# Performance work log

Hardware: AMD Instinct MI355X
Metric: run time of the kernel (lower is better)

## Reference

```python
import jax, jax.numpy as jnp
import numpy as np

N, T, F, H, DEG = 1024, 32, 128, 4, 32
HID, OUT = 512, 64
NNZ = N * DEG
D = F // H


def setup_inputs() -> dict:
    key = jax.random.key(0)
    ks = jax.random.split(key, 40)
    p = lambda i, shape, s=0.05: (jax.random.normal(ks[i], shape, dtype=jnp.float32) * s)
    inp = {
        'A_rows': jnp.repeat(jnp.arange(N, dtype=jnp.int32), DEG),
        'A_cols': jax.random.randint(ks[0], (NNZ,), 0, N, dtype=jnp.int32),
        'A_vals': jax.random.uniform(ks[1], (NNZ,), dtype=jnp.float32) / DEG,
        'X': jax.random.normal(ks[2], (N, T, F), dtype=jnp.float32),
        'W_gcn': p(3, (F, F)),
        'W_ih': p(4, (3 * F, F)), 'W_hh': p(5, (3 * F, F)),
        'b_ih': p(6, (3 * F,)), 'b_hh': p(7, (3 * F,)),
        'in_proj_w': p(8, (3 * F, F)), 'in_proj_b': p(9, (3 * F,)),
        'out_proj_w': p(10, (F, F)), 'out_proj_b': p(11, (F,)),
        'ln1_g': jnp.ones((F,), jnp.float32), 'ln1_b': jnp.zeros((F,), jnp.float32),
        'ln2_g': jnp.ones((F,), jnp.float32), 'ln2_b': jnp.zeros((F,), jnp.float32),
        'lnf_g': jnp.ones((F,), jnp.float32), 'lnf_b': jnp.zeros((F,), jnp.float32),
        'ff1_w': p(12, (HID, F)), 'ff1_b': p(13, (HID,)),
        'ff2_w': p(14, (F, HID)), 'ff2_b': p(15, (F,)),
        'fc1_w': p(16, (HID, T * F)), 'fc1_b': p(17, (HID,)),
        'fc2_w': p(18, (HID, HID)), 'fc2_b': p(19, (HID,)),
        'fc3_w': p(20, (OUT, HID)), 'fc3_b': p(21, (OUT,)),
    }
    return inp


def _pos_encoding():
    # pe[i, t] = sin(t / 10000**(2i/F)) for even t, cos(...) for odd t; constant over feature dim.
    i = jnp.arange(N, dtype=jnp.float32)
    t = jnp.arange(T, dtype=jnp.float32)
    inv = jnp.exp(-(2.0 * i / F) * jnp.log(jnp.float32(10000.0)))  # [N]
    ang = t[None, :] * inv[:, None]                                # [N, T]
    even = (jnp.arange(T) % 2 == 0)[None, :]
    return jnp.where(even, jnp.sin(ang), jnp.cos(ang))             # [N, T]


def _layer_norm(x, g, b, eps=1e-5):
    mu = x.mean(-1, keepdims=True)
    var = ((x - mu) ** 2).mean(-1, keepdims=True)
    return (x - mu) * jax.lax.rsqrt(var + eps) * g + b


def _forward(A_rows, A_cols, A_vals, X, W_gcn, W_ih, W_hh, b_ih, b_hh,
             in_proj_w, in_proj_b, out_proj_w, out_proj_b,
             ln1_g, ln1_b, ln2_g, ln2_b, lnf_g, lnf_b,
             ff1_w, ff1_b, ff2_w, ff2_b,
             fc1_w, fc1_b, fc2_w, fc2_b, fc3_w, fc3_b):
    def spmm(x2d):  # A_hat @ x2d via COO gather + segment-sum
        return jax.ops.segment_sum(A_vals[:, None] * x2d[A_cols], A_rows, num_segments=N)

    def gru_cell(x, h):  # torch GRUCell, gate order [r; z; n]
        gi = x @ W_ih.T + b_ih
        gh = h @ W_hh.T + b_hh
        ir, iz, inn = jnp.split(gi, 3, axis=-1)
        hr, hz, hn = jnp.split(gh, 3, axis=-1)
        r = jax.nn.sigmoid(ir + hr)
        z = jax.nn.sigmoid(iz + hz)
        n = jnp.tanh(inn + r * hn)
        return (1.0 - z) * n + z * h

    # GCN on full [N, T, F] block
    X_tilde = jax.nn.relu(spmm(X.reshape(N, T * F)).reshape(N, T, F) @ W_gcn)

    # sequential GRU + per-step GCN over time
    def step(h, x_t):
        g = gru_cell(x_t, h)                       # [N, F]
        h_new = jax.nn.relu(spmm(g) @ W_gcn)
        return h_new, g

    h0 = jnp.zeros((N, F), X.dtype)
    _, Hs = jax.lax.scan(step, h0, jnp.transpose(X_tilde, (1, 0, 2)))  # [T, N, F]
    Hm = jnp.transpose(Hs, (1, 0, 2)) + _pos_encoding()[:, :, None]    # [N, T, F]

    # TransformerEncoderLayer (post-norm, relu, dropout=0); seq axis = nodes, batch axis = T
    qkv = Hm @ in_proj_w.T + in_proj_b                 # [N, T, 3F]
    q, k, v = jnp.split(qkv, 3, axis=-1)
    q = q.reshape(N, T, H, D) * (1.0 / jnp.sqrt(jnp.float32(D)))
    k = k.reshape(N, T, H, D)
    v = v.reshape(N, T, H, D)
    scores = jnp.einsum('nthd,mthd->thnm', q, k)       # [T, H, N, N]
    attn = jax.nn.softmax(scores, axis=-1)
    ctx = jnp.einsum('thnm,mthd->nthd', attn, v).reshape(N, T, F)
    attn_out = ctx @ out_proj_w.T + out_proj_b
    x1 = _layer_norm(Hm + attn_out, ln1_g, ln1_b)
    ff = jax.nn.relu(x1 @ ff1_w.T + ff1_b) @ ff2_w.T + ff2_b
    x2 = _layer_norm(x1 + ff, ln2_g, ln2_b)
    enc = _layer_norm(x2, lnf_g, lnf_b)                # final encoder norm

    # MLP head
    flat = enc.reshape(N, T * F)
    h1 = jax.nn.relu(flat @ fc1_w.T + fc1_b)
    h2 = jax.nn.relu(h1 @ fc2_w.T + fc2_b)
    return h2 @ fc3_w.T + fc3_b                        # [N, OUT]


def reference(A_rows, A_cols, A_vals, X, W_gcn, W_ih, W_hh, b_ih, b_hh,
              in_proj_w, in_proj_b, out_proj_w, out_proj_b,
              ln1_g, ln1_b, ln2_g, ln2_b, lnf_g, lnf_b,
              ff1_w, ff1_b, ff2_w, ff2_b,
              fc1_w, fc1_b, fc2_w, fc2_b, fc3_w, fc3_b):
    return _forward(A_rows, A_cols, A_vals, X, W_gcn, W_ih, W_hh, b_ih, b_hh,
                    in_proj_w, in_proj_b, out_proj_w, out_proj_b,
                    ln1_g, ln1_b, ln2_g, ln2_b, lnf_g, lnf_b,
                    ff1_w, ff1_b, ff2_w, ff2_b,
                    fc1_w, fc1_b, fc2_w, fc2_b, fc3_w, fc3_b)
```

## Files before the change

kernel.cpp:

```cpp
#include <hip/hip_runtime.h>
#include <hip/hip_bf16.h>
#include <math.h>

#define N_NODES 1024
#define T_STEPS 32
#define F_DIM   128
#define H_HEADS 4
#define D_HEAD  32
#define DEG     32
#define HID     512
#define OUT_DIM 64
#define TF      (T_STEPS * F_DIM)
#define NT      (N_NODES * T_STEPS)
#define F3      (3 * F_DIM)

typedef __attribute__((ext_vector_type(8))) __bf16 bf16x8;
typedef __attribute__((ext_vector_type(4))) float  f32x4;

__device__ __forceinline__ short f2bf(float x) {
    union { float f; unsigned u; } v; v.f = x;
    unsigned r = (v.u + 0x7FFFu + ((v.u >> 16) & 1u)) >> 16;
    return (short)r;
}
__device__ __forceinline__ float bf2f(unsigned short b) {
    union { unsigned u; float f; } v; v.u = ((unsigned)b) << 16; return v.f;
}

__global__ void zero_kernel(float* p, int n) {
    int i = blockIdx.x * 256 + threadIdx.x;
    if (i < n) p[i] = 0.f;
}

template <bool RELU>
__global__ void bias_act(float* __restrict__ C, const float* __restrict__ bias,
                         int P, int total) {
    int i = blockIdx.x * 256 + threadIdx.x;
    if (i < total) {
        float v = C[i] + bias[i & (P - 1)];
        if (RELU) v = fmaxf(v, 0.f);
        C[i] = v;
    }
}

__global__ void prep_weights(const float* __restrict__ W_hh, const float* __restrict__ W_gcn,
                             unsigned short* __restrict__ WhhT_bf,
                             unsigned short* __restrict__ Wg_bf) {
    int idx = blockIdx.x * 256 + threadIdx.x;
    if (idx < F3 * F_DIM) {
        int j = idx / F_DIM;
        int k = idx % F_DIM;
        WhhT_bf[k * F3 + j] = (unsigned short)f2bf(W_hh[idx]);
    }
    if (idx < F_DIM * F_DIM) {
        Wg_bf[idx] = (unsigned short)f2bf(W_gcn[idx]);
    }
}

__global__ void spmm_wide(const int* __restrict__ cols, const float* __restrict__ vals,
                          const float* __restrict__ X, float* __restrict__ Y) {
    int n = blockIdx.y;
    int c = blockIdx.x * 256 + threadIdx.x;
    const int*   ce = cols + n * DEG;
    const float* ve = vals + n * DEG;
    float acc = 0.f;
#pragma unroll
    for (int e = 0; e < DEG; ++e) acc += ve[e] * X[ce[e] * TF + c];
    Y[n * TF + c] = acc;
}

__global__ __launch_bounds__(256) void gates0_kernel(
        const float* __restrict__ GI, const float* __restrict__ b_hh,
        float* __restrict__ g_out, float* __restrict__ Hm) {
    int idx = blockIdx.x * 256 + threadIdx.x;
    int n = idx >> 7, f = idx & 127;
    size_t gib = (size_t)n * T_STEPS * F3;
    float rr = 1.f / (1.f + expf(-(GI[gib + f] + b_hh[f])));
    float zz = 1.f / (1.f + expf(-(GI[gib + 128 + f] + b_hh[128 + f])));
    float nn = tanhf(GI[gib + 256 + f] + rr * b_hh[256 + f]);
    float g  = (1.f - zz) * nn;
    g_out[idx] = g;
    Hm[(size_t)n * T_STEPS * F_DIM + f] = g;
}

__global__ __launch_bounds__(256) void scan_step(
        const int* __restrict__ cols, const float* __restrict__ vals,
        const float* __restrict__ g_in, const unsigned short* __restrict__ Wg_bf,
        const unsigned short* __restrict__ WhhT_bf, const float* __restrict__ b_hh,
        const float* __restrict__ GI, float* __restrict__ g_out,
        float* __restrict__ Hm, int t_next) {
    __shared__ float sp[2][F_DIM];
    __shared__ float hsn[2][F_DIM];
    __shared__ float part[2][F_DIM][8];
    __shared__ float gpart[2][2][F_DIM];
    int tid = threadIdx.x;
    int n0 = blockIdx.x * 2;
    int f = tid & 127, half = tid >> 7;
    float b0 = 0.f, b1 = 0.f;
    int eb = half * 16;
#pragma unroll
    for (int e = 0; e < 16; ++e) {
        int i0 = n0 * DEG + eb + e;
        int i1 = (n0 + 1) * DEG + eb + e;
        b0 += vals[i0] * g_in[cols[i0] * F_DIM + f];
        b1 += vals[i1] * g_in[cols[i1] * F_DIM + f];
    }
    gpart[half][0][f] = b0; gpart[half][1][f] = b1;
    __syncthreads();
    sp[half][f] = gpart[0][half][f] + gpart[1][half][f];
    __syncthreads();
    float c0 = 0.f, c1 = 0.f;
    int kb = half * 64;
#pragma unroll 4
    for (int k = 0; k < 64; ++k) {
        int kk = kb + k;
        float w = bf2f(Wg_bf[kk * F_DIM + f]);
        c0 += sp[0][kk] * w; c1 += sp[1][kk] * w;
    }
    gpart[half][0][f] = c0; gpart[half][1][f] = c1;
    __syncthreads();
    hsn[half][f] = fmaxf(gpart[0][half][f] + gpart[1][half][f], 0.f);
    __syncthreads();
    float a[6] = {0.f, 0.f, 0.f, 0.f, 0.f, 0.f};
#pragma unroll 2
    for (int k = 0; k < 64; ++k) {
        int kk = kb + k;
        const unsigned short* w = WhhT_bf + kk * F3;
        float wr = bf2f(w[f]), wz = bf2f(w[128 + f]), wn = bf2f(w[256 + f]);
        float h0 = hsn[0][kk], h1 = hsn[1][kk];
        a[0] += h0 * wr; a[1] += h0 * wz; a[2] += h0 * wn;
        a[3] += h1 * wr; a[4] += h1 * wz; a[5] += h1 * wn;
    }
#pragma unroll
    for (int i = 0; i < 6; ++i) part[half][f][i] = a[i];
    __syncthreads();
    {
        int node = n0 + half;
        float ghr = part[0][f][half * 3 + 0] + part[1][f][half * 3 + 0] + b_hh[f];
        float ghz = part[0][f][half * 3 + 1] + part[1][f][half * 3 + 1] + b_hh[128 + f];
        float ghn = part[0][f][half * 3 + 2] + part[1][f][half * 3 + 2] + b_hh[256 + f];
        size_t gib = ((size_t)node * T_STEPS + t_next) * F3;
        float hv = hsn[half][f];
        float rr = 1.f / (1.f + expf(-(GI[gib + f] + ghr)));
        float zz = 1.f / (1.f + expf(-(GI[gib + 128 + f] + ghz)));
        float nn = tanhf(GI[gib + 256 + f] + rr * ghn);
        float g  = (1.f - zz) * nn + zz * hv;
        g_out[node * F_DIM + f] = g;
        float inv = __expf(-(float)node * (9.210340371976184f / 64.0f));
        float ang = (float)t_next * inv;
        float pe  = ((t_next & 1) == 0) ? sinf(ang) : cosf(ang);
        Hm[((size_t)node * T_STEPS + t_next) * F_DIM + f] = g + pe;
    }
}

#define GEMM128_STAGE(AP, BP, KDIM)                                              \
    _Pragma("unroll")                                                            \
    for (int i = 0; i < 4; ++i) {                                                \
        int idx = tid * 4 + i;                                                   \
        int r = idx >> 3, c4 = (idx & 7) << 2;                                   \
        const float4 f4 = *(const float4*)((AP) + (size_t)(row0 + r) * (KDIM) + k0 + c4); \
        union { __hip_bfloat162 h2[2]; short4 s4; } u;                           \
        u.h2[0] = __float22bfloat162_rn(make_float2(f4.x, f4.y));                \
        u.h2[1] = __float22bfloat162_rn(make_float2(f4.z, f4.w));                \
        *(short4*)&As[r][c4] = u.s4;                                             \
    }                                                                            \
    _Pragma("unroll")                                                            \
    for (int i = 0; i < 4; ++i) {                                                \
        int idx = tid * 4 + i;                                                   \
        int r = idx >> 3, c4 = (idx & 7) << 2;                                   \
        const float4 f4 = *(const float4*)((BP) + (size_t)(p0 + r) * (KDIM) + k0 + c4); \
        union { __hip_bfloat162 h2[2]; short4 s4; } u;                           \
        u.h2[0] = __float22bfloat162_rn(make_float2(f4.x, f4.y));                \
        u.h2[1] = __float22bfloat162_rn(make_float2(f4.z, f4.w));                \
        *(short4*)&Bs[r][c4] = u.s4;                                             \
    }

template <bool RELU>
__global__ __launch_bounds__(256) void mfma_gemm128(const float* __restrict__ A,
                                                    const float* __restrict__ B,
                                                    const float* __restrict__ bias,
                                                    float* __restrict__ C,
                                                    int M, int K, int P) {
    __shared__ short As[128][40];
    __shared__ short Bs[128][40];
    int tid = threadIdx.x;
    int p0 = blockIdx.x * 128, row0 = blockIdx.y * 128;
    int lane = tid & 63, w = tid >> 6, col = lane & 15, quad = lane >> 4;
    int qr = w >> 1, qc = w & 1;
    f32x4 acc[4][4];
#pragma unroll
    for (int j = 0; j < 4; ++j)
#pragma unroll
        for (int jj = 0; jj < 4; ++jj) acc[j][jj] = (f32x4){0.f, 0.f, 0.f, 0.f};

    for (int k0 = 0; k0 < K; k0 += 32) {
        GEMM128_STAGE(A, B, K)
        __syncthreads();
        bf16x8 af[4], bfr[4];
#pragma unroll
        for (int j = 0; j < 4; ++j) af[j]  = *(const bf16x8*)&As[qr * 64 + j * 16 + col][quad * 8];
#pragma unroll
        for (int j = 0; j < 4; ++j) bfr[j] = *(const bf16x8*)&Bs[qc * 64 + j * 16 + col][quad * 8];
#pragma unroll
        for (int j = 0; j < 4; ++j)
#pragma unroll
            for (int jj = 0; jj < 4; ++jj)
                acc[j][jj] = __builtin_amdgcn_mfma_f32_16x16x32_bf16(af[j], bfr[jj], acc[j][jj], 0, 0, 0);
        __syncthreads();
    }
#pragma unroll
    for (int j = 0; j < 4; ++j) {
#pragma unroll
        for (int jj = 0; jj < 4; ++jj) {
            int cg = p0 + qc * 64 + jj * 16 + col;
            float bvv = bias ? bias[cg] : 0.f;
#pragma unroll
            for (int r = 0; r < 4; ++r) {
                int rg = row0 + qr * 64 + j * 16 + quad * 4 + r;
                float v = acc[j][jj][r] + bvv;
                if (RELU) v = fmaxf(v, 0.f);
                C[(size_t)rg * P + cg] = v;
            }
        }
    }
}

__global__ __launch_bounds__(256) void qkv_gemm128(const float* __restrict__ A,
                                                   const float* __restrict__ B,
                                                   const float* __restrict__ bias,
                                                   short* __restrict__ Qb,
                                                   short* __restrict__ Kb,
                                                   short* __restrict__ VTb) {
    __shared__ short As[128][40];
    __shared__ short Bs[128][40];
    int tid = threadIdx.x;
    int p0 = blockIdx.x * 128, row0 = blockIdx.y * 128;
    int lane = tid & 63, w = tid >> 6, col = lane & 15, quad = lane >> 4;
    int qr = w >> 1, qc = w & 1;
    const int K = F_DIM;
    f32x4 acc[4][4];
#pragma unroll
    for (int j = 0; j < 4; ++j)
#pragma unroll
        for (int jj = 0; jj < 4; ++jj) acc[j][jj] = (f32x4){0.f, 0.f, 0.f, 0.f};

    for (int k0 = 0; k0 < K; k0 += 32) {
        GEMM128_STAGE(A, B, K)
        __syncthreads();
        bf16x8 af[4], bfr[4];
#pragma unroll
        for (int j = 0; j < 4; ++j) af[j]  = *(const bf16x8*)&As[qr * 64 + j * 16 + col][quad * 8];
#pragma unroll
        for (int j = 0; j < 4; ++j) bfr[j] = *(const bf16x8*)&Bs[qc * 64 + j * 16 + col][quad * 8];
#pragma unroll
        for (int j = 0; j < 4; ++j)
#pragma unroll
            for (int jj = 0; jj < 4; ++jj)
                acc[j][jj] = __builtin_amdgcn_mfma_f32_16x16x32_bf16(af[j], bfr[jj], acc[j][jj], 0, 0, 0);
        __syncthreads();
    }
#pragma unroll
    for (int j = 0; j < 4; ++j) {
#pragma unroll
        for (int jj = 0; jj < 4; ++jj) {
            int cg = p0 + qc * 64 + jj * 16 + col;
            int which = cg >> 7, f = cg & 127;
            int hh = f >> 5, d = f & 31;
            float bv = bias[cg];
#pragma unroll
            for (int r = 0; r < 4; ++r) {
                int rg = row0 + qr * 64 + j * 16 + quad * 4 + r;
                int n = rg >> 5, t = rg & 31;
                int th = t * H_HEADS + hh;
                float v = acc[j][jj][r] + bv;
                if (which == 0)
                    Qb[((size_t)th * N_NODES + n) * D_HEAD + d] = f2bf(v * 0.17677669529663687f);
                else if (which == 1)
                    Kb[((size_t)th * N_NODES + n) * D_HEAD + d] = f2bf(v);
                else
                    VTb[((size_t)th * D_HEAD + d) * N_NODES + n] = f2bf(v);
            }
        }
    }
}

__global__ __launch_bounds__(256) void attn_mfma(const short* __restrict__ Qb,
                                                 const short* __restrict__ Kb,
                                                 const short* __restrict__ VTb,
                                                 float* __restrict__ ctx) {
    int th = blockIdx.x;
    int t = th >> 2, hh = th & 3;
    int q0 = blockIdx.y * 64;
    int tid = threadIdx.x;
    int w = tid >> 6, lane = tid & 63;
    int col = lane & 15, quad = lane >> 4;
    __shared__ short    Ks[32][40];
    __shared__ short    Vs[32][40];
    __shared__ unsigned Ps[4][16][20];

    bf16x8 qf = *(const bf16x8*)(Qb + ((size_t)th * N_NODES + q0 + w * 16 + col) * D_HEAD + quad * 8);
    const short* Kbase = Kb  + (size_t)th * (N_NODES * D_HEAD);
    const short* Vbase = VTb + (size_t)th * (D_HEAD * N_NODES);

    int lrw = tid >> 3;
    int lc  = (tid & 7) * 4;
    int kperm = ((lrw & 15) << 1) | (lrw >> 4);

    f32x4 o0 = {0.f, 0.f, 0.f, 0.f}, o1 = {0.f, 0.f, 0.f, 0.f};
    float l0 = 0.f, l1 = 0.f, l2 = 0.f, l3 = 0.f;
    const f32x4 zc = {0.f, 0.f, 0.f, 0.f};

    for (int mt = 0; mt < 32; ++mt) {
        int m0 = mt * 32;
        __syncthreads();
        *(short4*)&Ks[lrw][lc] = *(const short4*)(Kbase + (size_t)(m0 + kperm) * D_HEAD + lc);
        *(short4*)&Vs[lrw][lc] = *(const short4*)(Vbase + (size_t)lrw * N_NODES + m0 + lc);
        __syncthreads();
        bf16x8 k0 = *(const bf16x8*)&Ks[col][quad * 8];
        bf16x8 k1 = *(const bf16x8*)&Ks[col + 16][quad * 8];
        f32x4 s0 = __builtin_amdgcn_mfma_f32_16x16x32_bf16(qf, k0, zc, 0, 0, 0);
        f32x4 s1 = __builtin_amdgcn_mfma_f32_16x16x32_bf16(qf, k1, zc, 0, 0, 0);
        float ps[4][2];
#pragma unroll
        for (int r = 0; r < 4; ++r) {
            ps[r][0] = __expf(fminf(s0[r], 80.f));
            ps[r][1] = __expf(fminf(s1[r], 80.f));
            union { __hip_bfloat162 h; unsigned u; } u;
            u.h = __float22bfloat162_rn(make_float2(ps[r][0], ps[r][1]));
            Ps[w][quad * 4 + r][col] = u.u;
        }
        l0 += ps[0][0] + ps[0][1]; l1 += ps[1][0] + ps[1][1];
        l2 += ps[2][0] + ps[2][1]; l3 += ps[3][0] + ps[3][1];
        __builtin_amdgcn_s_waitcnt(0xC07F);
        bf16x8 pf = *(const bf16x8*)&Ps[w][col][quad * 4];
        bf16x8 v0 = *(const bf16x8*)&Vs[col][quad * 8];
        bf16x8 v1 = *(const bf16x8*)&Vs[col + 16][quad * 8];
        o0 = __builtin_amdgcn_mfma_f32_16x16x32_bf16(pf, v0, o0, 0, 0, 0);
        o1 = __builtin_amdgcn_mfma_f32_16x16x32_bf16(pf, v1, o1, 0, 0, 0);
    }
    float lr[4] = {l0, l1, l2, l3};
#pragma unroll
    for (int r = 0; r < 4; ++r) {
        float s = lr[r];
        s += __shfl_xor(s, 1); s += __shfl_xor(s, 2);
        s += __shfl_xor(s, 4); s += __shfl_xor(s, 8);
        lr[r] = 1.f / s;
    }
#pragma unroll
    for (int r = 0; r < 4; ++r) {
        int n = q0 + w * 16 + quad * 4 + r;
        size_t base = ((size_t)n * T_STEPS + t) * F_DIM + hh * D_HEAD;
        ctx[base + col]      = o0[r] * lr[r];
        ctx[base + 16 + col] = o1[r] * lr[r];
    }
}

__global__ __launch_bounds__(256) void ln_kernel(
        const float* __restrict__ a, const float* __restrict__ resid,
        const float* __restrict__ gamma, const float* __restrict__ beta,
        float* __restrict__ out) {
    int row = blockIdx.x * 4 + (threadIdx.x >> 6);
    int tid = threadIdx.x & 63;
    int base = row * F_DIM;
    float x0 = a[base + tid], x1 = a[base + 64 + tid];
    if (resid) { x0 += resid[base + tid]; x1 += resid[base + 64 + tid]; }
    float s = x0 + x1;
#pragma unroll
    for (int o = 32; o > 0; o >>= 1) s += __shfl_xor(s, o);
    float mu = s * (1.f / 128.f);
    float d0 = x0 - mu, d1 = x1 - mu;
    float v = d0 * d0 + d1 * d1;
#pragma unroll
    for (int o = 32; o > 0; o >>= 1) v += __shfl_xor(v, o);
    float inv = rsqrtf(v * (1.f / 128.f) + 1e-5f);
    out[base + tid]      = d0 * inv * gamma[tid] + beta[tid];
    out[base + 64 + tid] = d1 * inv * gamma[64 + tid] + beta[64 + tid];
}

template <bool TB, bool RELU, bool SPLITK>
__global__ __launch_bounds__(256) void mfma_gemm(const float* __restrict__ A,
                                                 const float* __restrict__ B,
                                                 const float* __restrict__ bias,
                                                 float* __restrict__ C,
                                                 int M, int K, int P, int Kc) {
    __shared__ short As[64][40];
    __shared__ short Bs[64][40];
    int tid = threadIdx.x;
    int p0 = blockIdx.x * 64, row0 = blockIdx.y * 64;
    int k_begin = SPLITK ? blockIdx.z * Kc : 0;
    int k_end   = SPLITK ? k_begin + Kc : K;
    int lane = tid & 63, w = tid >> 6, col = lane & 15, quad = lane >> 4;
    f32x4 acc[4];
#pragma unroll
    for (int j = 0; j < 4; ++j) acc[j] = (f32x4){0.f, 0.f, 0.f, 0.f};

    for (int k0 = k_begin; k0 < k_end; k0 += 32) {
#pragma unroll
        for (int i = 0; i < 2; ++i) {
            int idx = tid * 2 + i;
            int r = idx >> 3, c4 = (idx & 7) << 2;
            const float4 f4 = *(const float4*)(A + (size_t)(row0 + r) * K + k0 + c4);
            union { __hip_bfloat162 h2[2]; short4 s4; } u;
            u.h2[0] = __float22bfloat162_rn(make_float2(f4.x, f4.y));
            u.h2[1] = __float22bfloat162_rn(make_float2(f4.z, f4.w));
            *(short4*)&As[r][c4] = u.s4;
        }
        if (TB) {
#pragma unroll
            for (int i = 0; i < 2; ++i) {
                int idx = tid * 2 + i;
                int r = idx >> 3, c4 = (idx & 7) << 2;
                const float4 f4 = *(const float4*)(B + (size_t)(p0 + r) * K + k0 + c4);
                union { __hip_bfloat162 h2[2]; short4 s4; } u;
                u.h2[0] = __float22bfloat162_rn(make_float2(f4.x, f4.y));
                u.h2[1] = __float22bfloat162_rn(make_float2(f4.z, f4.w));
                *(short4*)&Bs[r][c4] = u.s4;
            }
        } else {
#pragma unroll
            for (int i = 0; i < 2; ++i) {
                int idx = tid * 2 + i;
                int kk = idx >> 4, c4 = (idx & 15) << 2;
                const float4 f4 = *(const float4*)(B + (size_t)(k0 + kk) * P + p0 + c4);
                Bs[c4 + 0][kk] = f2bf(f4.x);
                Bs[c4 + 1][kk] = f2bf(f4.y);
                Bs[c4 + 2][kk] = f2bf(f4.z);
                Bs[c4 + 3][kk] = f2bf(f4.w);
            }
        }
        __syncthreads();
        bf16x8 af = *(const bf16x8*)&As[w * 16 + col][quad * 8];
#pragma unroll
        for (int j = 0; j < 4; ++j) {
            bf16x8 bv = *(const bf16x8*)&Bs[j * 16 + col][quad * 8];
            acc[j] = __builtin_amdgcn_mfma_f32_16x16x32_bf16(af, bv, acc[j], 0, 0, 0);
        }
        __syncthreads();
    }
#pragma unroll
    for (int j = 0; j < 4; ++j) {
        int cg_ = p0 + j * 16 + col;
        float bvv = (!SPLITK && bias) ? bias[cg_] : 0.f;
#pragma unroll
        for (int r = 0; r < 4; ++r) {
            int rg = row0 + w * 16 + quad * 4 + r;
            if (SPLITK) {
                atomicAdd(&C[(size_t)rg * P + cg_], acc[j][r]);
            } else {
                float v = acc[j][r] + bvv;
                if (RELU) v = fmaxf(v, 0.f);
                C[(size_t)rg * P + cg_] = v;
            }
        }
    }
}

extern "C" void kernel_launch(void* const* d_in, const int* in_sizes, int n_in,
                              void* d_out, int out_size, void* d_ws, size_t ws_size,
                              hipStream_t stream) {
    const int*   A_cols     = (const int*)d_in[1];
    const float* A_vals     = (const float*)d_in[2];
    const float* X          = (const float*)d_in[3];
    const float* W_gcn      = (const float*)d_in[4];
    const float* W_ih       = (const float*)d_in[5];
    const float* W_hh       = (const float*)d_in[6];
    const float* b_ih       = (const float*)d_in[7];
    const float* b_hh       = (const float*)d_in[8];
    const float* in_proj_w  = (const float*)d_in[9];
    const float* in_proj_b  = (const float*)d_in[10];
    const float* out_proj_w = (const float*)d_in[11];
    const float* out_proj_b = (const float*)d_in[12];
    const float* ln1_g = (const float*)d_in[13];
    const float* ln1_b = (const float*)d_in[14];
    const float* ln2_g = (const float*)d_in[15];
    const float* ln2_b = (const float*)d_in[16];
    const float* lnf_g = (const float*)d_in[17];
    const float* lnf_b = (const float*)d_in[18];
    const float* ff1_w = (const float*)d_in[19];
    const float* ff1_b = (const float*)d_in[20];
    const float* ff2_w = (const float*)d_in[21];
    const float* ff2_b = (const float*)d_in[22];
    const float* fc1_w = (const float*)d_in[23];
    const float* fc1_b = (const float*)d_in[24];
    const float* fc2_w = (const float*)d_in[25];
    const float* fc2_b = (const float*)d_in[26];
    const float* fc3_w = (const float*)d_in[27];
    const float* fc3_b = (const float*)d_in[28];
    float* out = (float*)d_out;
    float* ws  = (float*)d_ws;

    const size_t o_Hm = 0;
    const size_t o_A  = o_Hm + 4194304;
    const size_t o_B  = o_A + 4194304;
    const size_t o_C  = o_B + 4194304;
    const size_t o_D  = o_C + 12582912;
    const size_t o_WT = o_D + 12582912;
    const size_t o_h  = o_WT + 49152;
    const size_t o_g  = o_h + 131072;
    const size_t o_h1 = o_g + 131072;
    const size_t o_h2 = o_h1 + 524288;

    float* Hm    = ws + o_Hm;
    float* bufA  = ws + o_A;
    float* bufB  = ws + o_B;
    float* bufC  = ws + o_C;
    short* Qb    = (short*)(ws + o_D);
    short* Kb    = Qb + 4194304;
    short* VTb   = Kb + 4194304;
    unsigned short* WhhT_bf = (unsigned short*)(ws + o_WT);
    unsigned short* Wg_bf   = WhhT_bf + 49152;
    float* g0    = ws + o_g;
    float* h1    = ws + o_h1;
    float* h2    = ws + o_h2;
    float* g1    = h2;

    spmm_wide<<<dim3(16, 1024), 256, 0, stream>>>(A_cols, A_vals, X, bufA);
    mfma_gemm<false, true, false><<<dim3(2, 512), 256, 0, stream>>>(bufA, W_gcn, nullptr, bufB, NT, F_DIM, F_DIM, 0);
    mfma_gemm128<false><<<dim3(3, 256), 256, 0, stream>>>(bufB, W_ih, b_ih, bufC, NT, F_DIM, F3);
    prep_weights<<<192, 256, 0, stream>>>(W_hh, W_gcn, WhhT_bf, Wg_bf);
    gates0_kernel<<<512, 256, 0, stream>>>(bufC, b_hh, g0, Hm);
    for (int s = 0; s < T_STEPS - 1; ++s) {
        const float* gi = (s & 1) ? g1 : g0;
        float*       go = (s & 1) ? g0 : g1;
        scan_step<<<512, 256, 0, stream>>>(A_cols, A_vals, gi, Wg_bf, WhhT_bf, b_hh, bufC, go, Hm, s + 1);
    }
    qkv_gemm128<<<dim3(3, 256), 256, 0, stream>>>(Hm, in_proj_w, in_proj_b, Qb, Kb, VTb);
    attn_mfma<<<dim3(128, 16), 256, 0, stream>>>(Qb, Kb, VTb, bufA);
    mfma_gemm<true, false, false><<<dim3(2, 512), 256, 0, stream>>>(bufA, out_proj_w, out_proj_b, bufB, NT, F_DIM, F_DIM, 0);
    ln_kernel<<<NT / 4, 256, 0, stream>>>(Hm, bufB, ln1_g, ln1_b, bufA);
    mfma_gemm128<true><<<dim3(4, 256), 256, 0, stream>>>(bufA, ff1_w, ff1_b, bufC, NT, F_DIM, HID);
    mfma_gemm128<false><<<dim3(1, 256), 256, 0, stream>>>(bufC, ff2_w, ff2_b, bufB, NT, HID, F_DIM);
    ln_kernel<<<NT / 4, 256, 0, stream>>>(bufA, bufB, ln2_g, ln2_b, Hm);
    ln_kernel<<<NT / 4, 256, 0, stream>>>(Hm, nullptr, lnf_g, lnf_b, bufA);
    zero_kernel<<<2048, 256, 0, stream>>>(h1, 524288);
    mfma_gemm<true, false, true><<<dim3(8, 16, 4), 256, 0, stream>>>(bufA, fc1_w, nullptr, h1, N_NODES, TF, HID, 1024);
    bias_act<true><<<2048, 256, 0, stream>>>(h1, fc1_b, HID, 524288);
    zero_kernel<<<2048, 256, 0, stream>>>(h2, 524288);
    mfma_gemm<true, false, true><<<dim3(8, 16, 4), 256, 0, stream>>>(h1, fc2_w, nullptr, h2, N_NODES, HID, HID, 128);
    bias_act<true><<<2048, 256, 0, stream>>>(h2, fc2_b, HID, 524288);
    zero_kernel<<<256, 256, 0, stream>>>(out, 65536);
    mfma_gemm<true, false, true><<<dim3(1, 16, 8), 256, 0, stream>>>(h2, fc3_w, nullptr, out, N_NODES, HID, OUT_DIM, 64);
    bias_act<false><<<256, 256, 0, stream>>>(out, fc3_b, OUT_DIM, 65536);
}
```

Baseline: 779.0 us.

## Store FFN hidden in bf16 and transpose V in a separate tiled kernel

The FF1 GEMM now writes its ReLU output as bf16, and FF2 loads that bf16 activation directly. This halves the intermediate traffic and removes a float-to-bf16 conversion in FF2's staging. The QKV GEMM now writes V in the same row-major layout as Q and K, replacing its scattered transposed stores. A new shared-memory tile kernel then produces the transposed V, at the cost of one extra launch and one extra pass over V.

```diff
diff --git a/kernel.cpp b/kernel.cpp
--- a/kernel.cpp
+++ b/kernel.cpp
@@ -152,33 +152,11 @@
     }
 }
 
-#define GEMM128_STAGE(AP, BP, KDIM)                                              \
-    _Pragma("unroll")                                                            \
-    for (int i = 0; i < 4; ++i) {                                                \
-        int idx = tid * 4 + i;                                                   \
-        int r = idx >> 3, c4 = (idx & 7) << 2;                                   \
-        const float4 f4 = *(const float4*)((AP) + (size_t)(row0 + r) * (KDIM) + k0 + c4); \
-        union { __hip_bfloat162 h2[2]; short4 s4; } u;                           \
-        u.h2[0] = __float22bfloat162_rn(make_float2(f4.x, f4.y));                \
-        u.h2[1] = __float22bfloat162_rn(make_float2(f4.z, f4.w));                \
-        *(short4*)&As[r][c4] = u.s4;                                             \
-    }                                                                            \
-    _Pragma("unroll")                                                            \
-    for (int i = 0; i < 4; ++i) {                                                \
-        int idx = tid * 4 + i;                                                   \
-        int r = idx >> 3, c4 = (idx & 7) << 2;                                   \
-        const float4 f4 = *(const float4*)((BP) + (size_t)(p0 + r) * (KDIM) + k0 + c4); \
-        union { __hip_bfloat162 h2[2]; short4 s4; } u;                           \
-        u.h2[0] = __float22bfloat162_rn(make_float2(f4.x, f4.y));                \
-        u.h2[1] = __float22bfloat162_rn(make_float2(f4.z, f4.w));                \
-        *(short4*)&Bs[r][c4] = u.s4;                                             \
-    }
-
-template <bool RELU>
-__global__ __launch_bounds__(256) void mfma_gemm128(const float* __restrict__ A,
+template <bool RELU, bool ABF16, bool BF16OUT>
+__global__ __launch_bounds__(256) void mfma_gemm128(const void* __restrict__ Aptr,
                                                     const float* __restrict__ B,
                                                     const float* __restrict__ bias,
-                                                    float* __restrict__ C,
+                                                    void* __restrict__ Cptr,
                                                     int M, int K, int P) {
     __shared__ short As[128][40];
     __shared__ short Bs[128][40];
@@ -193,7 +171,37 @@
         for (int jj = 0; jj < 4; ++jj) acc[j][jj] = (f32x4){0.f, 0.f, 0.f, 0.f};
 
     for (int k0 = 0; k0 < K; k0 += 32) {
-        GEMM128_STAGE(A, B, K)
+        if (ABF16) {
+            const short* A = (const short*)Aptr;
+#pragma unroll
+            for (int i = 0; i < 2; ++i) {
+                int idx = tid * 2 + i;
+                int r = idx >> 2, c8 = (idx & 3) * 8;
+                *(int4*)&As[r][c8] = *(const int4*)(A + (size_t)(row0 + r) * K + k0 + c8);
+            }
+        } else {
+            const float* A = (const float*)Aptr;
+#pragma unroll
+            for (int i = 0; i < 4; ++i) {
+                int idx = tid * 4 + i;
+                int r = idx >> 3, c4 = (idx & 7) << 2;
+                const float4 f4 = *(const float4*)(A + (size_t)(row0 + r) * K + k0 + c4);
+                union { __hip_bfloat162 h2[2]; short4 s4; } u;
+                u.h2[0] = __float22bfloat162_rn(make_float2(f4.x, f4.y));
+                u.h2[1] = __float22bfloat162_rn(make_float2(f4.z, f4.w));
+                *(short4*)&As[r][c4] = u.s4;
+            }
+        }
+#pragma unroll
+        for (int i = 0; i < 4; ++i) {
+            int idx = tid * 4 + i;
+            int r = idx >> 3, c4 = (idx & 7) << 2;
+            const float4 f4 = *(const float4*)(B + (size_t)(p0 + r) * K + k0 + c4);
+            union { __hip_bfloat162 h2[2]; short4 s4; } u;
+            u.h2[0] = __float22bfloat162_rn(make_float2(f4.x, f4.y));
+            u.h2[1] = __float22bfloat162_rn(make_float2(f4.z, f4.w));
+            *(short4*)&Bs[r][c4] = u.s4;
+        }
         __syncthreads();
         bf16x8 af[4], bfr[4];
 #pragma unroll
@@ -218,7 +226,8 @@
                 int rg = row0 + qr * 64 + j * 16 + quad * 4 + r;
                 float v = acc[j][jj][r] + bvv;
                 if (RELU) v = fmaxf(v, 0.f);
-                C[(size_t)rg * P + cg] = v;
+                if (BF16OUT) ((short*)Cptr)[(size_t)rg * P + cg] = f2bf(v);
+                else         ((float*)Cptr)[(size_t)rg * P + cg] = v;
             }
         }
     }
@@ -229,7 +238,7 @@
                                                    const float* __restrict__ bias,
                                                    short* __restrict__ Qb,
                                                    short* __restrict__ Kb,
-                                                   short* __restrict__ VTb) {
+                                                   short* __restrict__ Vb) {
     __shared__ short As[128][40];
     __shared__ short Bs[128][40];
     int tid = threadIdx.x;
@@ -244,7 +253,26 @@
         for (int jj = 0; jj < 4; ++jj) acc[j][jj] = (f32x4){0.f, 0.f, 0.f, 0.f};
 
     for (int k0 = 0; k0 < K; k0 += 32) {
-        GEMM128_STAGE(A, B, K)
+#pragma unroll
+        for (int i = 0; i < 4; ++i) {
+            int idx = tid * 4 + i;
+            int r = idx >> 3, c4 = (idx & 7) << 2;
+            const float4 f4 = *(const float4*)(A + (size_t)(row0 + r) * K + k0 + c4);
+            union { __hip_bfloat162 h2[2]; short4 s4; } u;
+            u.h2[0] = __float22bfloat162_rn(make_float2(f4.x, f4.y));
+            u.h2[1] = __float22bfloat162_rn(make_float2(f4.z, f4.w));
+            *(short4*)&As[r][c4] = u.s4;
+        }
+#pragma unroll
+        for (int i = 0; i < 4; ++i) {
+            int idx = tid * 4 + i;
+            int r = idx >> 3, c4 = (idx & 7) << 2;
+            const float4 f4 = *(const float4*)(B + (size_t)(p0 + r) * K + k0 + c4);
+            union { __hip_bfloat162 h2[2]; short4 s4; } u;
+            u.h2[0] = __float22bfloat162_rn(make_float2(f4.x, f4.y));
+            u.h2[1] = __float22bfloat162_rn(make_float2(f4.z, f4.w));
+            *(short4*)&Bs[r][c4] = u.s4;
+        }
         __syncthreads();
         bf16x8 af[4], bfr[4];
 #pragma unroll
@@ -271,15 +299,34 @@
                 int rg = row0 + qr * 64 + j * 16 + quad * 4 + r;
                 int n = rg >> 5, t = rg & 31;
                 int th = t * H_HEADS + hh;
+                size_t dst = ((size_t)th * N_NODES + n) * D_HEAD + d;
                 float v = acc[j][jj][r] + bv;
-                if (which == 0)
-                    Qb[((size_t)th * N_NODES + n) * D_HEAD + d] = f2bf(v * 0.17677669529663687f);
-                else if (which == 1)
-                    Kb[((size_t)th * N_NODES + n) * D_HEAD + d] = f2bf(v);
-                else
-                    VTb[((size_t)th * D_HEAD + d) * N_NODES + n] = f2bf(v);
-            }
-        }
+                if (which == 0)      Qb[dst] = f2bf(v * 0.17677669529663687f);
+                else if (which == 1) Kb[dst] = f2bf(v);
+                else                 Vb[dst] = f2bf(v);
+            }
+        }
+    }
+}
+
+__global__ __launch_bounds__(256) void vtrans(const short* __restrict__ Vb,
+                                              short* __restrict__ VTb) {
+    __shared__ short tile[32][36];
+    int th = blockIdx.x;
+    int n0 = blockIdx.y * 32;
+    int tid = threadIdx.x;
+    {
+        int n_i = tid >> 3, d0 = (tid & 7) * 4;
+        *(short4*)&tile[n_i][d0] =
+            *(const short4*)(Vb + ((size_t)th * N_NODES + n0 + n_i) * D_HEAD + d0);
+    }
+    __syncthreads();
+    {
+        int d = tid >> 3, m0 = (tid & 7) * 4;
+        short4 o;
+        o.x = tile[m0 + 0][d]; o.y = tile[m0 + 1][d];
+        o.z = tile[m0 + 2][d]; o.w = tile[m0 + 3][d];
+        *(short4*)(VTb + ((size_t)th * D_HEAD + d) * N_NODES + n0 + m0) = o;
     }
 }
 
@@ -503,9 +550,11 @@
     float* bufA  = ws + o_A;
     float* bufB  = ws + o_B;
     float* bufC  = ws + o_C;
+    short* ffh   = (short*)bufC;
     short* Qb    = (short*)(ws + o_D);
     short* Kb    = Qb + 4194304;
     short* VTb   = Kb + 4194304;
+    short* Vb    = VTb + 4194304;
     unsigned short* WhhT_bf = (unsigned short*)(ws + o_WT);
     unsigned short* Wg_bf   = WhhT_bf + 49152;
     float* g0    = ws + o_g;
@@ -515,7 +564,7 @@
 
     spmm_wide<<<dim3(16, 1024), 256, 0, stream>>>(A_cols, A_vals, X, bufA);
     mfma_gemm<false, true, false><<<dim3(2, 512), 256, 0, stream>>>(bufA, W_gcn, nullptr, bufB, NT, F_DIM, F_DIM, 0);
-    mfma_gemm128<false><<<dim3(3, 256), 256, 0, stream>>>(bufB, W_ih, b_ih, bufC, NT, F_DIM, F3);
+    mfma_gemm128<false, false, false><<<dim3(3, 256), 256, 0, stream>>>(bufB, W_ih, b_ih, bufC, NT, F_DIM, F3);
     prep_weights<<<192, 256, 0, stream>>>(W_hh, W_gcn, WhhT_bf, Wg_bf);
     gates0_kernel<<<512, 256, 0, stream>>>(bufC, b_hh, g0, Hm);
     for (int s = 0; s < T_STEPS - 1; ++s) {
@@ -523,12 +572,13 @@
         float*       go = (s & 1) ? g0 : g1;
         scan_step<<<512, 256, 0, stream>>>(A_cols, A_vals, gi, Wg_bf, WhhT_bf, b_hh, bufC, go, Hm, s + 1);
     }
-    qkv_gemm128<<<dim3(3, 256), 256, 0, stream>>>(Hm, in_proj_w, in_proj_b, Qb, Kb, VTb);
+    qkv_gemm128<<<dim3(3, 256), 256, 0, stream>>>(Hm, in_proj_w, in_proj_b, Qb, Kb, Vb);
+    vtrans<<<dim3(128, 32), 256, 0, stream>>>(Vb, VTb);
     attn_mfma<<<dim3(128, 16), 256, 0, stream>>>(Qb, Kb, VTb, bufA);
     mfma_gemm<true, false, false><<<dim3(2, 512), 256, 0, stream>>>(bufA, out_proj_w, out_proj_b, bufB, NT, F_DIM, F_DIM, 0);
     ln_kernel<<<NT / 4, 256, 0, stream>>>(Hm, bufB, ln1_g, ln1_b, bufA);
-    mfma_gemm128<true><<<dim3(4, 256), 256, 0, stream>>>(bufA, ff1_w, ff1_b, bufC, NT, F_DIM, HID);
-    mfma_gemm128<false><<<dim3(1, 256), 256, 0, stream>>>(bufC, ff2_w, ff2_b, bufB, NT, HID, F_DIM);
+    mfma_gemm128<true, false, true><<<dim3(4, 256), 256, 0, stream>>>(bufA, ff1_w, ff1_b, ffh, NT, F_DIM, HID);
+    mfma_gemm128<false, true, false><<<dim3(1, 256), 256, 0, stream>>>(ffh, ff2_w, ff2_b, bufB, NT, HID, F_DIM);
     ln_kernel<<<NT / 4, 256, 0, stream>>>(bufA, bufB, ln2_g, ln2_b, Hm);
     ln_kernel<<<NT / 4, 256, 0, stream>>>(Hm, nullptr, lnf_g, lnf_b, bufA);
     zero_kernel<<<2048, 256, 0, stream>>>(h1, 524288);
```

New measurement: 738.3 us. -5.2%, faster.
